# Optimization experiments

Hardware: AMD Instinct MI355X
Metric: run time of the kernel (lower is better)

## Reference

```python
import jax, jax.numpy as jnp
import numpy as np

OPS = jnp.array([[1,1,1],[1,1,-1],[1,-1,1],[1,-1,-1],[-1,1,1],[-1,1,-1],[-1,-1,1],[-1,-1,-1]], dtype=jnp.float32)  # [8,3] sign flips per eigenvector column

B, N, FN, FE, E = 1, 512, 8, 1, 32
D0 = 6 + FN  # layer-0 node embedding dim: framed (x,v) = 6 dims + node features


def setup_inputs() -> dict:
    key = jax.random.key(0)
    ks = jax.random.split(key, 24)
    rn = lambda k, shp, s=0.1: jax.random.normal(k, shp, jnp.float32) * s
    inp = {
        'node_feat': jax.random.normal(ks[0], (B, N, FN), jnp.float32),
        'edge_feat': jax.random.normal(ks[1], (B, N, N, FE), jnp.float32),
        'x': jax.random.normal(ks[2], (B, N, 3), jnp.float32),
        'v': jax.random.normal(ks[3], (B, N, 3), jnp.float32),
        # GNN layer 0 (input node dim D0)
        'e0_w1': rn(ks[4], (FE + 2 * D0, E)), 'e0_b1': jnp.zeros((E,), jnp.float32),
        'e0_w2': rn(ks[5], (E, E)), 'e0_b2': jnp.zeros((E,), jnp.float32),
        'n0_w1': rn(ks[6], (D0 + E, E)), 'n0_b1': jnp.zeros((E,), jnp.float32),
        'n0_w2': rn(ks[7], (E, E)), 'n0_b2': jnp.zeros((E,), jnp.float32),
        # GNN layer 1 (input node dim E)
        'e1_w1': rn(ks[8], (FE + 2 * E, E)), 'e1_b1': jnp.zeros((E,), jnp.float32),
        'e1_w2': rn(ks[9], (E, E)), 'e1_b2': jnp.zeros((E,), jnp.float32),
        'n1_w1': rn(ks[10], (E + E, E)), 'n1_b1': jnp.zeros((E,), jnp.float32),
        'n1_w2': rn(ks[11], (E, E)), 'n1_b2': jnp.zeros((E,), jnp.float32),
        # decoder: relu -> Linear(E,E) -> relu -> Linear(E,6)
        'dec_w1': rn(ks[12], (E, E)), 'dec_b1': jnp.zeros((E,), jnp.float32),
        'dec_w2': rn(ks[13], (E, 6)), 'dec_b2': jnp.zeros((6,), jnp.float32),
        # v_coef: relu -> Linear(E,E) -> relu -> Linear(E,1)
        'vc_w1': rn(ks[14], (E, E)), 'vc_b1': jnp.zeros((E,), jnp.float32),
        'vc_w2': rn(ks[15], (E, 1)), 'vc_b2': jnp.zeros((1,), jnp.float32),
    }
    return inp


def _gnn_layer(h, edge_feat, ew1, eb1, ew2, eb2, nw1, nb1, nw2, nb2):
    # h: [B,N,d]; edge_feat: [B,N,N,Fe]
    # Torch builds concat([edge_feat, h_j, h_i]) per (i,j) pair; we split W1 rows
    # to avoid materializing the [B,N,N,Fe+2d] concat (same math).
    Fe = edge_feat.shape[-1]
    d = h.shape[-1]
    pre_e = edge_feat @ ew1[:Fe]          # [B,N,N,E]
    pre_j = h @ ew1[Fe:Fe + d]            # [B,N,E], indexed by j
    pre_i = h @ ew1[Fe + d:]              # [B,N,E], indexed by i
    m = jax.nn.relu(pre_e + pre_j[:, None, :, :] + pre_i[:, :, None, :] + eb1)
    m = jax.nn.relu(m @ ew2 + eb2)        # [B,N,N,E]
    agg = m.sum(axis=2)                   # sum over neighbors j -> [B,N,E]
    dn = jax.nn.relu(h @ nw1[:d] + agg @ nw1[d:] + nb1)
    return dn @ nw2 + nb2                 # [B,N,E]


def reference(node_feat, edge_feat, x, v,
              e0_w1, e0_b1, e0_w2, e0_b2, n0_w1, n0_b1, n0_w2, n0_b2,
              e1_w1, e1_b1, e1_w2, e1_b2, n1_w1, n1_b1, n1_w2, n1_b2,
              dec_w1, dec_b1, dec_w2, dec_b2, vc_w1, vc_b1, vc_w2, vc_b2):
    # ---- create_frame (PCA frame averaging) ----
    center = x.mean(axis=1, keepdims=True)                 # [B,1,3]
    xc = x - center
    R = jnp.einsum('bni,bnj->bij', xc, xc)                 # [B,3,3]
    _, Vv = jnp.linalg.eigh(R)                             # eigenvectors, ascending (like torch.symeig)
    F_ops = jax.lax.stop_gradient(OPS[None, :, None, :] * Vv[:, None, :, :])  # [B,8,3,3]
    center = jax.lax.stop_gradient(center)
    xc = x - center
    fx = jnp.einsum('boji,bnj->obni', F_ops, xc)           # [8,B,N,3] (F_ops^T applied)
    fv = jnp.einsum('boji,bnj->obni', F_ops, v)            # [8,B,N,3]
    nf = jnp.broadcast_to(node_feat[None], (8,) + node_feat.shape)
    h0 = jnp.concatenate([fx, fv, nf], axis=-1)            # [8,B,N,6+FN]

    l0 = (e0_w1, e0_b1, e0_w2, e0_b2, n0_w1, n0_b1, n0_w2, n0_b2)
    l1 = (e1_w1, e1_b1, e1_w2, e1_b2, n1_w1, n1_b1, n1_w2, n1_b2)
    frames = []
    for i in range(8):  # small fixed frame count; loop keeps N^2 intermediates per-frame
        hi = _gnn_layer(h0[i], edge_feat, *l0)
        hi = _gnn_layer(hi, edge_feat, *l1)
        frames.append(hi)
    h_out = jnp.stack(frames)                              # [8,B,N,E]

    # ---- decoder + invert_frame ----
    s = jax.nn.relu(jax.nn.relu(h_out) @ dec_w1 + dec_b1)
    spatial_out = s @ dec_w2 + dec_b2                      # [8,B,N,6]
    so = jnp.transpose(spatial_out, (1, 0, 2, 3))          # [B,8,N,6]
    dx = jnp.einsum('boij,bonj->bni', F_ops, so[..., :3]) / 8.0
    dv = jnp.einsum('boij,bonj->bni', F_ops, so[..., 3:]) / 8.0

    h_mean = h_out.mean(axis=0)                            # [B,N,E]
    coef = jax.nn.relu(jax.nn.relu(h_mean) @ vc_w1 + vc_b1) @ vc_w2 + vc_b2  # [B,N,1]
    v_out = v + dv
    x_out = x + v_out * coef + dx
    return (h_mean, edge_feat, x_out, v_out)
```

## Files before the change

### kernel.cpp

```cpp
#include <hip/hip_runtime.h>
#include <hip/hip_bf16.h>
#include <hip/hip_fp16.h>
#include <math.h>

#define NN 512

typedef _Float16 f16x8 __attribute__((ext_vector_type(8)));
typedef float    f32x4 __attribute__((ext_vector_type(4)));

__device__ __forceinline__ void compute_frame(const float* __restrict__ x,
                                              float* __restrict__ sFR,
                                              double (*red)[9]) {
    const int t = threadIdx.x;
    double s[9] = {0,0,0,0,0,0,0,0,0};
    for (int n = t; n < NN; n += 256) {
        double X = x[n*3+0], Y = x[n*3+1], Z = x[n*3+2];
        s[0]+=X; s[1]+=Y; s[2]+=Z;
        s[3]+=X*X; s[4]+=X*Y; s[5]+=X*Z; s[6]+=Y*Y; s[7]+=Y*Z; s[8]+=Z*Z;
    }
    #pragma unroll
    for (int m = 1; m < 64; m <<= 1) {
        #pragma unroll
        for (int q = 0; q < 9; ++q) s[q] += __shfl_xor(s[q], m);
    }
    const int wave = t >> 6, lane = t & 63;
    if (lane == 0) {
        #pragma unroll
        for (int q = 0; q < 9; ++q) red[wave][q] = s[q];
    }
    __syncthreads();
    if (t == 0) {
        double S[9];
        #pragma unroll
        for (int q = 0; q < 9; ++q) S[q] = red[0][q]+red[1][q]+red[2][q]+red[3][q];
        double cx = S[0]/512.0, cy = S[1]/512.0, cz = S[2]/512.0;
        double A[3][3];
        A[0][0]=S[3]-512.0*cx*cx; A[0][1]=S[4]-512.0*cx*cy; A[0][2]=S[5]-512.0*cx*cz;
        A[1][1]=S[6]-512.0*cy*cy; A[1][2]=S[7]-512.0*cy*cz; A[2][2]=S[8]-512.0*cz*cz;
        A[1][0]=A[0][1]; A[2][0]=A[0][2]; A[2][1]=A[1][2];
        double V[3][3] = {{1,0,0},{0,1,0},{0,0,1}};
        for (int sweep = 0; sweep < 8; ++sweep) {
            double off = fabs(A[0][1]) + fabs(A[0][2]) + fabs(A[1][2]);
            double dia = fabs(A[0][0]) + fabs(A[1][1]) + fabs(A[2][2]);
            if (off < 1e-14 * (dia + 1e-300)) break;
            for (int p = 0; p < 3; ++p) for (int q = p+1; q < 3; ++q) {
                double apq = A[p][q];
                if (fabs(apq) < 1e-300) continue;
                double tau = (A[q][q] - A[p][p]) / (2.0 * apq);
                double tt = (tau >= 0 ? 1.0 : -1.0) / (fabs(tau) + sqrt(1.0 + tau*tau));
                double cc = 1.0 / sqrt(1.0 + tt*tt), ss = tt * cc;
                A[p][p] = A[p][p] - tt * apq;
                A[q][q] = A[q][q] + tt * apq;
                A[p][q] = 0.0; A[q][p] = 0.0;
                for (int k = 0; k < 3; ++k) if (k != p && k != q) {
                    double akp = A[k][p], akq = A[k][q];
                    A[k][p] = cc*akp - ss*akq; A[p][k] = A[k][p];
                    A[k][q] = ss*akp + cc*akq; A[q][k] = A[k][q];
                }
                for (int k = 0; k < 3; ++k) {
                    double vkp = V[k][p], vkq = V[k][q];
                    V[k][p] = cc*vkp - ss*vkq;
                    V[k][q] = ss*vkp + cc*vkq;
                }
            }
        }
        double ev[3] = {A[0][0], A[1][1], A[2][2]};
        int idx[3] = {0,1,2};
        for (int a = 0; a < 2; ++a) for (int b = a+1; b < 3; ++b)
            if (ev[idx[b]] < ev[idx[a]]) { int tmp = idx[a]; idx[a] = idx[b]; idx[b] = tmp; }
        sFR[0] = (float)cx; sFR[1] = (float)cy; sFR[2] = (float)cz;
        for (int r = 0; r < 3; ++r)
            for (int c = 0; c < 3; ++c)
                sFR[3 + r*3 + c] = (float)V[r][idx[c]];
    }
    __syncthreads();
}

__global__ void __launch_bounds__(256) pre0_kernel(
    const float* __restrict__ x, const float* __restrict__ v,
    const float* __restrict__ nf,
    const float* __restrict__ e0w1, const float* __restrict__ e0b1,
    const float* __restrict__ e0w2, const float* __restrict__ e1w1,
    const float* __restrict__ e1w2,
    const float* __restrict__ edge,
    float* __restrict__ FRg, float* __restrict__ H0,
    _Float16* __restrict__ PJF, _Float16* __restrict__ PIH,
    _Float16* __restrict__ WEH0, _Float16* __restrict__ WEH1,
    _Float16* __restrict__ W2F0, _Float16* __restrict__ W2F1,
    float* __restrict__ out_edge)
{
    __shared__ double red[4][9];
    __shared__ float sFR[12];
    const int t = threadIdx.x;
    const int b = blockIdx.x;

    compute_frame(x, sFR, red);

    ((float2*)out_edge)[b * 256 + t] = ((const float2*)edge)[b * 256 + t];

    if (b == 0) {
        const int lane = t & 63, wv = t >> 6;
        if (t < 12) FRg[t] = sFR[t];
        const int l15 = lane & 15, kb = (lane >> 4) * 8;
        if (wv == 1) {
            #pragma unroll
            for (int e = 0; e < 8; ++e) {
                W2F0[lane*16 + e]     = (_Float16)e0w2[(kb+e)*32 + l15];
                W2F0[lane*16 + 8 + e] = (_Float16)e0w2[(kb+e)*32 + l15 + 16];
            }
        } else if (wv == 2) {
            #pragma unroll
            for (int e = 0; e < 8; ++e) {
                W2F1[lane*16 + e]     = (_Float16)e1w2[(kb+e)*32 + l15];
                W2F1[lane*16 + 8 + e] = (_Float16)e1w2[(kb+e)*32 + l15 + 16];
            }
        } else if (wv == 3 && lane < 32) {
            WEH0[lane] = (_Float16)e0w1[lane];
            WEH1[lane] = (_Float16)e1w1[lane];
        }
    }

    const int c = t & 31;
    const int row = b * 8 + (t >> 5);
    const int o = row >> 9, j = row & 511;
    float hrow[14];
    float xc0 = x[j*3+0] - sFR[0], xc1 = x[j*3+1] - sFR[1], xc2 = x[j*3+2] - sFR[2];
    float v0 = v[j*3+0], v1 = v[j*3+1], v2 = v[j*3+2];
    #pragma unroll
    for (int i = 0; i < 3; ++i) {
        float sgn = ((o >> (2 - i)) & 1) ? -1.f : 1.f;
        float px = sFR[3 + 0*3 + i]*xc0 + sFR[3 + 1*3 + i]*xc1 + sFR[3 + 2*3 + i]*xc2;
        float pv = sFR[3 + 0*3 + i]*v0  + sFR[3 + 1*3 + i]*v1  + sFR[3 + 2*3 + i]*v2;
        hrow[i]     = sgn * px;
        hrow[3 + i] = sgn * pv;
    }
    #pragma unroll
    for (int k = 0; k < 8; ++k) hrow[6 + k] = nf[j*8 + k];
    if (c < 14) H0[row * 14 + c] = hrow[c];
    float pj = 0.f, pi = e0b1[c];
    #pragma unroll
    for (int k = 0; k < 14; ++k) {
        pj = fmaf(hrow[k], e0w1[(1 + k) * 32 + c], pj);
        pi = fmaf(hrow[k], e0w1[(15 + k) * 32 + c], pi);
    }
    PIH[row * 32 + c] = (_Float16)pi;
    const int fl = (j & 15) | ((c >> 3) << 4);
    PJF[(((o << 5) + (j >> 4)) * 64 + fl) * 8 + (c & 7)] = (_Float16)pj;
}

template<int D, bool NEXT>
__global__ void __launch_bounds__(256, 4) edge_kernel(
    const _Float16* __restrict__ PJF,
    const _Float16* __restrict__ PIH,
    const _Float16* __restrict__ WEH,
    const _Float16* __restrict__ W2F,
    const float* __restrict__ edge,
    const float* __restrict__ h,
    const float* __restrict__ eb2,
    const float* __restrict__ nw1,
    const float* __restrict__ nb1,
    const float* __restrict__ nw2,
    const float* __restrict__ nb2,
    float* __restrict__ hout,
    const float* __restrict__ ew1n,
    const float* __restrict__ eb1n,
    _Float16* __restrict__ PJFn,
    _Float16* __restrict__ PIn)
{
    const int t = threadIdx.x;
    const int wv = t >> 6, lane = t & 63;
    const int o = blockIdx.x >> 8;
    const int i0 = (blockIdx.x & 255) << 1;
    const int i = i0 + (wv & 1);
    const int jh = wv >> 1;
    const int row = (o << 9) | i;
    const int l15 = lane & 15;
    const int kbase = (lane >> 4) * 8;

    __shared__ float sAgg[4][32];

    const f16x8 pi8 = *(const f16x8*)(PIH + row * 32 + kbase);
    const f16x8 we8 = *(const f16x8*)(WEH + kbase);
    const f16x8 bfrag0 = *(const f16x8*)(W2F + lane * 16);
    const f16x8 bfrag1 = *(const f16x8*)(W2F + lane * 16 + 8);
    const float b2v0 = eb2[l15], b2v1 = eb2[l15 + 16];
    const f16x8 z8 = {0,0,0,0,0,0,0,0};
    float agg0 = 0.f, agg1 = 0.f;

    const float* edge_i = edge + (i << 9);
    const _Float16* pjf_o = PJF + (size_t)o * 16384;

    #pragma unroll
    for (int jm = 0; jm < 16; ++jm) {
        const int tile = (jh << 4) | jm;
        const f16x8 pj8 = *(const f16x8*)(pjf_o + (tile * 64 + lane) * 8);
        const _Float16 eh = (_Float16)edge_i[tile * 16 + l15];
        const f16x8 e8 = {eh, eh, eh, eh, eh, eh, eh, eh};
        f16x8 m = e8 * we8 + (pj8 + pi8);
        m = __builtin_elementwise_max(m, z8);
        f32x4 c0 = {0.f, 0.f, 0.f, 0.f};
        c0 = __builtin_amdgcn_mfma_f32_16x16x32_f16(m, bfrag0, c0, 0, 0, 0);
        #pragma unroll
        for (int r = 0; r < 4; ++r) agg0 += fmaxf(c0[r] + b2v0, 0.f);
        f32x4 c1 = {0.f, 0.f, 0.f, 0.f};
        c1 = __builtin_amdgcn_mfma_f32_16x16x32_f16(m, bfrag1, c1, 0, 0, 0);
        #pragma unroll
        for (int r = 0; r < 4; ++r) agg1 += fmaxf(c1[r] + b2v1, 0.f);
    }
    agg0 += __shfl_xor(agg0, 16); agg0 += __shfl_xor(agg0, 32);
    agg1 += __shfl_xor(agg1, 16); agg1 += __shfl_xor(agg1, 32);
    if (lane < 16) { sAgg[wv][l15] = agg0; sAgg[wv][16 + l15] = agg1; }
    __syncthreads();
    if (wv >= 2) return;

    const int c2 = lane & 31;
    const float red2 = sAgg[wv][c2] + sAgg[wv + 2][c2];
    const float* hr = h + row * D;
    float acc = nb1[c2];
    #pragma unroll
    for (int k = 0; k < D; ++k) acc = fmaf(hr[k], nw1[k * 32 + c2], acc);
    #pragma unroll
    for (int k = 0; k < 32; ++k)
        acc = fmaf(__shfl(red2, k, 32), nw1[(D + k) * 32 + c2], acc);
    const float dn = fmaxf(acc, 0.f);
    float outv = nb2[c2];
    #pragma unroll
    for (int k = 0; k < 32; ++k)
        outv = fmaf(__shfl(dn, k, 32), nw2[k * 32 + c2], outv);
    if (lane < 32) hout[row * 32 + c2] = outv;

    if (NEXT) {
        float pj1 = 0.f, pi1 = eb1n[c2];
        #pragma unroll
        for (int k = 0; k < 32; ++k) {
            const float hk = __shfl(outv, k, 32);
            pj1 = fmaf(hk, ew1n[(1 + k) * 32 + c2], pj1);
            pi1 = fmaf(hk, ew1n[(33 + k) * 32 + c2], pi1);
        }
        if (lane < 32) {
            PIn[row * 32 + c2] = (_Float16)pi1;
            const int fl = (i & 15) | ((c2 >> 3) << 4);
            PJFn[(((o << 5) + (i >> 4)) * 64 + fl) * 8 + (c2 & 7)] = (_Float16)pj1;
        }
    }
}

__global__ void __launch_bounds__(256) decfinal_kernel(
    const float* __restrict__ h2,
    const float* __restrict__ w1, const float* __restrict__ b1,
    const float* __restrict__ w2,
    const float* __restrict__ b2,
    const float* __restrict__ x, const float* __restrict__ v,
    const float* __restrict__ FR,
    const float* __restrict__ vw1, const float* __restrict__ vb1,
    const float* __restrict__ vw2, const float* __restrict__ vb2,
    float* __restrict__ out_hmean, float* __restrict__ out_x,
    float* __restrict__ out_v)
{
    const int n = blockIdx.x;
    const int t = threadIdx.x;
    const int wv = t >> 6, lane = t & 63;
    const int c = lane & 31;
    __shared__ float sSo[8][6];

    #pragma unroll
    for (int q = 0; q < 2; ++q) {
        const int o = (wv << 1) | q;
        const int row = (o << 9) | n;
        float rh = fmaxf(h2[row * 32 + c], 0.f);
        float acc = b1[c];
        #pragma unroll
        for (int k = 0; k < 32; ++k)
            acc = fmaf(__shfl(rh, k, 32), w1[k * 32 + c], acc);
        float s = fmaxf(acc, 0.f);
        #pragma unroll
        for (int m = 0; m < 6; ++m) {
            float p = s * w2[c * 6 + m];
            p += __shfl_xor(p, 1); p += __shfl_xor(p, 2); p += __shfl_xor(p, 4);
            p += __shfl_xor(p, 8); p += __shfl_xor(p, 16);
            if (lane == 0) sSo[o][m] = p + b2[m];
        }
    }
    __syncthreads();
    if (wv) return;

    float hm = 0.f;
    #pragma unroll
    for (int o = 0; o < 8; ++o) hm += h2[((o << 9) | n) * 32 + c];
    hm *= 0.125f;
    if (lane < 32) out_hmean[n * 32 + c] = hm;
    float rh = fmaxf(hm, 0.f);
    float acc = vb1[c];
    #pragma unroll
    for (int k = 0; k < 32; ++k)
        acc = fmaf(__shfl(rh, k, 32), vw1[k * 32 + c], acc);
    float t1 = fmaxf(acc, 0.f);
    float p = t1 * vw2[c];
    p += __shfl_xor(p, 1); p += __shfl_xor(p, 2); p += __shfl_xor(p, 4);
    p += __shfl_xor(p, 8); p += __shfl_xor(p, 16);
    float coef = p + vb2[0];
    if (lane < 3) {
        int i = lane;
        float dx = 0.f, dv = 0.f;
        #pragma unroll
        for (int o = 0; o < 8; ++o) {
            #pragma unroll
            for (int j = 0; j < 3; ++j) {
                float sgn = ((o >> (2 - j)) & 1) ? -1.f : 1.f;
                float f = sgn * FR[3 + i * 3 + j];
                dx = fmaf(f, sSo[o][j], dx);
                dv = fmaf(f, sSo[o][3 + j], dv);
            }
        }
        dx *= 0.125f; dv *= 0.125f;
        float vout = v[n * 3 + i] + dv;
        out_v[n * 3 + i] = vout;
        out_x[n * 3 + i] = x[n * 3 + i] + vout * coef + dx;
    }
}

extern "C" void kernel_launch(void* const* d_in, const int* in_sizes, int n_in,
                              void* d_out, int out_size, void* d_ws, size_t ws_size,
                              hipStream_t stream) {
    const float* node_feat = (const float*)d_in[0];
    const float* edge      = (const float*)d_in[1];
    const float* x         = (const float*)d_in[2];
    const float* v         = (const float*)d_in[3];
    const float* e0_w1 = (const float*)d_in[4];
    const float* e0_b1 = (const float*)d_in[5];
    const float* e0_w2 = (const float*)d_in[6];
    const float* e0_b2 = (const float*)d_in[7];
    const float* n0_w1 = (const float*)d_in[8];
    const float* n0_b1 = (const float*)d_in[9];
    const float* n0_w2 = (const float*)d_in[10];
    const float* n0_b2 = (const float*)d_in[11];
    const float* e1_w1 = (const float*)d_in[12];
    const float* e1_b1 = (const float*)d_in[13];
    const float* e1_w2 = (const float*)d_in[14];
    const float* e1_b2 = (const float*)d_in[15];
    const float* n1_w1 = (const float*)d_in[16];
    const float* n1_b1 = (const float*)d_in[17];
    const float* n1_w2 = (const float*)d_in[18];
    const float* n1_b2 = (const float*)d_in[19];
    const float* dec_w1 = (const float*)d_in[20];
    const float* dec_b1 = (const float*)d_in[21];
    const float* dec_w2 = (const float*)d_in[22];
    const float* dec_b2 = (const float*)d_in[23];
    const float* vc_w1 = (const float*)d_in[24];
    const float* vc_b1 = (const float*)d_in[25];
    const float* vc_w2 = (const float*)d_in[26];
    const float* vc_b2 = (const float*)d_in[27];

    char* wsb = (char*)d_ws;
    float* out = (float*)d_out;

    float*    FR   = (float*)wsb;
    float*    H0   = (float*)(wsb + 256);
    float*    HA   = (float*)(wsb + 256 + 229376);
    float*    HB   = (float*)(wsb + 256 + 229376 + 524288);
    char*     p    = wsb + 256 + 229376 + 524288 + 524288;
    _Float16* PJF0 = (_Float16*)p;            p += 262144;
    _Float16* PIH0 = (_Float16*)p;            p += 262144;
    _Float16* PJF1 = (_Float16*)p;            p += 262144;
    _Float16* PIH1 = (_Float16*)p;            p += 262144;
    _Float16* WEH0 = (_Float16*)p;            p += 256;
    _Float16* WEH1 = (_Float16*)p;            p += 256;
    _Float16* W2F0 = (_Float16*)p;            p += 2048;
    _Float16* W2F1 = (_Float16*)p;            p += 2048;

    pre0_kernel<<<512, 256, 0, stream>>>(x, v, node_feat,
                                         e0_w1, e0_b1, e0_w2, e1_w1, e1_w2,
                                         edge, FR, H0, PJF0, PIH0,
                                         WEH0, WEH1, W2F0, W2F1, out + 16384);
    edge_kernel<14, true><<<2048, 256, 0, stream>>>(
        PJF0, PIH0, WEH0, W2F0, edge, H0, e0_b2, n0_w1, n0_b1, n0_w2, n0_b2,
        HA, e1_w1, e1_b1, PJF1, PIH1);
    edge_kernel<32, false><<<2048, 256, 0, stream>>>(
        PJF1, PIH1, WEH1, W2F1, edge, HA, e1_b2, n1_w1, n1_b1, n1_w2, n1_b2,
        HB, nullptr, nullptr, nullptr, nullptr);
    decfinal_kernel<<<512, 256, 0, stream>>>(HB, dec_w1, dec_b1, dec_w2, dec_b2,
                                             x, v, FR, vc_w1, vc_b1, vc_w2, vc_b2,
                                             out, out + 278528, out + 280064);
}
```

Measured before the change: 154.9 us.

## Fuse all stages into one persistent kernel with software grid barriers

Replaces the four kernel launches with one 512-block kernel whose stages are separated by an atomic-counter grid barrier, removing launch gaps and inter-kernel drain. Each wave now handles two node rows over all 512 neighbours, sharing the PJF loads between them instead of splitting neighbours across waves and reducing through LDS. The barrier relies on all 512 blocks being resident at once (launch bounds of 3 blocks per CU), so it can deadlock if they are not co-resident. It also leaves fewer blocks in flight for latency hiding during the edge phases.

Result: slower. 366.8 us (+136.7%).

```diff
diff --git a/kernel.cpp b/kernel.cpp
--- a/kernel.cpp
+++ b/kernel.cpp
@@ -1,12 +1,53 @@
 #include <hip/hip_runtime.h>
-#include <hip/hip_bf16.h>
 #include <hip/hip_fp16.h>
 #include <math.h>
 
 #define NN 512
+#define NBLK 512
 
 typedef _Float16 f16x8 __attribute__((ext_vector_type(8)));
 typedef float    f32x4 __attribute__((ext_vector_type(4)));
+
+struct Params {
+    const float *x, *v, *nf;
+    const float *e0w1, *e0b1, *e0w2, *e0b2;
+    const float *n0w1, *n0b1, *n0w2, *n0b2;
+    const float *e1w1, *e1b1, *e1w2, *e1b2;
+    const float *n1w1, *n1b1, *n1w2, *n1b2;
+    const float *dw1, *db1, *dw2, *db2;
+    const float *vw1, *vb1, *vw2, *vb2;
+    const float *edge;
+    float *FR, *H0, *HA, *HB;
+    _Float16 *PJF0, *PIH0, *PJF1, *PIH1;
+    _Float16 *WEH0, *WEH1, *W2F0, *W2F1;
+    float *out_hmean, *out_edge, *out_x, *out_v;
+};
+
+__device__ unsigned g_bar_cnt = 0;
+__device__ unsigned g_bar_gen = 0;
+
+__device__ __forceinline__ void grid_sync() {
+    __syncthreads();
+    if (threadIdx.x == 0) {
+        __threadfence();
+        unsigned my = __hip_atomic_load(&g_bar_gen, __ATOMIC_RELAXED,
+                                        __HIP_MEMORY_SCOPE_AGENT);
+        unsigned prev = __hip_atomic_fetch_add(&g_bar_cnt, 1u, __ATOMIC_ACQ_REL,
+                                               __HIP_MEMORY_SCOPE_AGENT);
+        if (prev == (unsigned)(NBLK - 1)) {
+            __hip_atomic_store(&g_bar_cnt, 0u, __ATOMIC_RELAXED,
+                               __HIP_MEMORY_SCOPE_AGENT);
+            __hip_atomic_store(&g_bar_gen, my + 1u, __ATOMIC_RELEASE,
+                               __HIP_MEMORY_SCOPE_AGENT);
+        } else {
+            while (__hip_atomic_load(&g_bar_gen, __ATOMIC_RELAXED,
+                                     __HIP_MEMORY_SCOPE_AGENT) == my)
+                __builtin_amdgcn_s_sleep(2);
+        }
+        __threadfence();
+    }
+    __syncthreads();
+}
 
 __device__ __forceinline__ void compute_frame(const float* __restrict__ x,
                                               float* __restrict__ sFR,
@@ -76,80 +117,56 @@
     __syncthreads();
 }
 
-__global__ void __launch_bounds__(256) pre0_kernel(
-    const float* __restrict__ x, const float* __restrict__ v,
-    const float* __restrict__ nf,
-    const float* __restrict__ e0w1, const float* __restrict__ e0b1,
-    const float* __restrict__ e0w2, const float* __restrict__ e1w1,
-    const float* __restrict__ e1w2,
-    const float* __restrict__ edge,
-    float* __restrict__ FRg, float* __restrict__ H0,
-    _Float16* __restrict__ PJF, _Float16* __restrict__ PIH,
-    _Float16* __restrict__ WEH0, _Float16* __restrict__ WEH1,
-    _Float16* __restrict__ W2F0, _Float16* __restrict__ W2F1,
-    float* __restrict__ out_edge)
+template<int D, bool NEXT>
+__device__ __forceinline__ void node_tail(
+    const int row, const float agg0, const float agg1,
+    const float* __restrict__ h,
+    const float* __restrict__ nw1, const float* __restrict__ nb1,
+    const float* __restrict__ nw2, const float* __restrict__ nb2,
+    float* __restrict__ hout,
+    const float* __restrict__ ew1n, const float* __restrict__ eb1n,
+    _Float16* __restrict__ PJFn, _Float16* __restrict__ PIn)
 {
-    __shared__ double red[4][9];
-    __shared__ float sFR[12];
-    const int t = threadIdx.x;
-    const int b = blockIdx.x;
-
-    compute_frame(x, sFR, red);
-
-    ((float2*)out_edge)[b * 256 + t] = ((const float2*)edge)[b * 256 + t];
-
-    if (b == 0) {
-        const int lane = t & 63, wv = t >> 6;
-        if (t < 12) FRg[t] = sFR[t];
-        const int l15 = lane & 15, kb = (lane >> 4) * 8;
-        if (wv == 1) {
-            #pragma unroll
-            for (int e = 0; e < 8; ++e) {
-                W2F0[lane*16 + e]     = (_Float16)e0w2[(kb+e)*32 + l15];
-                W2F0[lane*16 + 8 + e] = (_Float16)e0w2[(kb+e)*32 + l15 + 16];
-            }
-        } else if (wv == 2) {
-            #pragma unroll
-            for (int e = 0; e < 8; ++e) {
-                W2F1[lane*16 + e]     = (_Float16)e1w2[(kb+e)*32 + l15];
-                W2F1[lane*16 + 8 + e] = (_Float16)e1w2[(kb+e)*32 + l15 + 16];
-            }
-        } else if (wv == 3 && lane < 32) {
-            WEH0[lane] = (_Float16)e0w1[lane];
-            WEH1[lane] = (_Float16)e1w1[lane];
-        }
-    }
-
-    const int c = t & 31;
-    const int row = b * 8 + (t >> 5);
-    const int o = row >> 9, j = row & 511;
-    float hrow[14];
-    float xc0 = x[j*3+0] - sFR[0], xc1 = x[j*3+1] - sFR[1], xc2 = x[j*3+2] - sFR[2];
-    float v0 = v[j*3+0], v1 = v[j*3+1], v2 = v[j*3+2];
+    const int lane = threadIdx.x & 63;
+    const int c2 = lane & 31;
+    const float* hr = h + row * D;
+    float acc = nb1[c2];
     #pragma unroll
-    for (int i = 0; i < 3; ++i) {
-        float sgn = ((o >> (2 - i)) & 1) ? -1.f : 1.f;
-        float px = sFR[3 + 0*3 + i]*xc0 + sFR[3 + 1*3 + i]*xc1 + sFR[3 + 2*3 + i]*xc2;
-        float pv = sFR[3 + 0*3 + i]*v0  + sFR[3 + 1*3 + i]*v1  + sFR[3 + 2*3 + i]*v2;
-        hrow[i]     = sgn * px;
-        hrow[3 + i] = sgn * pv;
-    }
+    for (int k = 0; k < D; ++k) acc = fmaf(hr[k], nw1[k * 32 + c2], acc);
     #pragma unroll
-    for (int k = 0; k < 8; ++k) hrow[6 + k] = nf[j*8 + k];
-    if (c < 14) H0[row * 14 + c] = hrow[c];
-    float pj = 0.f, pi = e0b1[c];
+    for (int k = 0; k < 16; ++k)
+        acc = fmaf(__shfl(agg0, k, 32), nw1[(D + k) * 32 + c2], acc);
     #pragma unroll
-    for (int k = 0; k < 14; ++k) {
-        pj = fmaf(hrow[k], e0w1[(1 + k) * 32 + c], pj);
-        pi = fmaf(hrow[k], e0w1[(15 + k) * 32 + c], pi);
-    }
-    PIH[row * 32 + c] = (_Float16)pi;
-    const int fl = (j & 15) | ((c >> 3) << 4);
-    PJF[(((o << 5) + (j >> 4)) * 64 + fl) * 8 + (c & 7)] = (_Float16)pj;
+    for (int k = 0; k < 16; ++k)
+        acc = fmaf(__shfl(agg1, k, 32), nw1[(D + 16 + k) * 32 + c2], acc);
+    const float dn = fmaxf(acc, 0.f);
+    float outv = nb2[c2];
+    #pragma unroll
+    for (int k = 0; k < 32; ++k)
+        outv = fmaf(__shfl(dn, k, 32), nw2[k * 32 + c2], outv);
+    if (lane < 32) hout[row * 32 + c2] = outv;
+
+    if (NEXT) {
+        float pj1 = 0.f, pi1 = eb1n[c2];
+        #pragma unroll
+        for (int k = 0; k < 32; ++k) {
+            const float hk = __shfl(outv, k, 32);
+            pj1 = fmaf(hk, ew1n[(1 + k) * 32 + c2], pj1);
+            pi1 = fmaf(hk, ew1n[(33 + k) * 32 + c2], pi1);
+        }
+        if (lane < 32) {
+            PIn[row * 32 + c2] = (_Float16)pi1;
+            const int i = row & 511;
+            const int o = row >> 9;
+            const int fl = (i & 15) | ((c2 >> 3) << 4);
+            PJFn[(((o << 5) + (i >> 4)) * 64 + fl) * 8 + (c2 & 7)] = (_Float16)pj1;
+        }
+    }
 }
 
 template<int D, bool NEXT>
-__global__ void __launch_bounds__(256, 4) edge_kernel(
+__device__ __forceinline__ void edge_phase2(
+    const int o, const int i0,
     const _Float16* __restrict__ PJF,
     const _Float16* __restrict__ PIH,
     const _Float16* __restrict__ WEH,
@@ -157,228 +174,259 @@
     const float* __restrict__ edge,
     const float* __restrict__ h,
     const float* __restrict__ eb2,
-    const float* __restrict__ nw1,
-    const float* __restrict__ nb1,
-    const float* __restrict__ nw2,
-    const float* __restrict__ nb2,
+    const float* __restrict__ nw1, const float* __restrict__ nb1,
+    const float* __restrict__ nw2, const float* __restrict__ nb2,
     float* __restrict__ hout,
-    const float* __restrict__ ew1n,
-    const float* __restrict__ eb1n,
-    _Float16* __restrict__ PJFn,
-    _Float16* __restrict__ PIn)
+    const float* __restrict__ ew1n, const float* __restrict__ eb1n,
+    _Float16* __restrict__ PJFn, _Float16* __restrict__ PIn)
 {
+    const int lane = threadIdx.x & 63;
+    const int l15 = lane & 15;
+    const int kbase = (lane >> 4) * 8;
+    const int row0 = (o << 9) | i0;
+    const int row1 = row0 + 1;
+
+    const f16x8 piA = *(const f16x8*)(PIH + row0 * 32 + kbase);
+    const f16x8 piB = *(const f16x8*)(PIH + row1 * 32 + kbase);
+    const f16x8 we8 = *(const f16x8*)(WEH + kbase);
+    const f16x8 bf0 = *(const f16x8*)(W2F + lane * 16);
+    const f16x8 bf1 = *(const f16x8*)(W2F + lane * 16 + 8);
+    const float b2v0 = eb2[l15], b2v1 = eb2[l15 + 16];
+    const f16x8 z8 = {0,0,0,0,0,0,0,0};
+    float aggA0 = 0.f, aggA1 = 0.f, aggB0 = 0.f, aggB1 = 0.f;
+
+    const float* eA = edge + (i0 << 9);
+    const float* eB = eA + 512;
+    const _Float16* pjf_o = PJF + (size_t)o * 16384;
+
+    #pragma unroll 4
+    for (int tile = 0; tile < 32; ++tile) {
+        const f16x8 pj8 = *(const f16x8*)(pjf_o + (tile * 64 + lane) * 8);
+        const _Float16 ehA = (_Float16)eA[tile * 16 + l15];
+        const _Float16 ehB = (_Float16)eB[tile * 16 + l15];
+        const f16x8 eA8 = {ehA, ehA, ehA, ehA, ehA, ehA, ehA, ehA};
+        const f16x8 eB8 = {ehB, ehB, ehB, ehB, ehB, ehB, ehB, ehB};
+        f16x8 mA = eA8 * we8 + (pj8 + piA);
+        mA = __builtin_elementwise_max(mA, z8);
+        f16x8 mB = eB8 * we8 + (pj8 + piB);
+        mB = __builtin_elementwise_max(mB, z8);
+        f32x4 c;
+        c = (f32x4){0.f,0.f,0.f,0.f};
+        c = __builtin_amdgcn_mfma_f32_16x16x32_f16(mA, bf0, c, 0, 0, 0);
+        #pragma unroll
+        for (int r = 0; r < 4; ++r) aggA0 += fmaxf(c[r] + b2v0, 0.f);
+        c = (f32x4){0.f,0.f,0.f,0.f};
+        c = __builtin_amdgcn_mfma_f32_16x16x32_f16(mA, bf1, c, 0, 0, 0);
+        #pragma unroll
+        for (int r = 0; r < 4; ++r) aggA1 += fmaxf(c[r] + b2v1, 0.f);
+        c = (f32x4){0.f,0.f,0.f,0.f};
+        c = __builtin_amdgcn_mfma_f32_16x16x32_f16(mB, bf0, c, 0, 0, 0);
+        #pragma unroll
+        for (int r = 0; r < 4; ++r) aggB0 += fmaxf(c[r] + b2v0, 0.f);
+        c = (f32x4){0.f,0.f,0.f,0.f};
+        c = __builtin_amdgcn_mfma_f32_16x16x32_f16(mB, bf1, c, 0, 0, 0);
+        #pragma unroll
+        for (int r = 0; r < 4; ++r) aggB1 += fmaxf(c[r] + b2v1, 0.f);
+    }
+    aggA0 += __shfl_xor(aggA0, 16); aggA0 += __shfl_xor(aggA0, 32);
+    aggA1 += __shfl_xor(aggA1, 16); aggA1 += __shfl_xor(aggA1, 32);
+    aggB0 += __shfl_xor(aggB0, 16); aggB0 += __shfl_xor(aggB0, 32);
+    aggB1 += __shfl_xor(aggB1, 16); aggB1 += __shfl_xor(aggB1, 32);
+
+    node_tail<D, NEXT>(row0, aggA0, aggA1, h, nw1, nb1, nw2, nb2, hout,
+                       ew1n, eb1n, PJFn, PIn);
+    node_tail<D, NEXT>(row1, aggB0, aggB1, h, nw1, nb1, nw2, nb2, hout,
+                       ew1n, eb1n, PJFn, PIn);
+}
+
+__global__ void __launch_bounds__(256, 3) fused_kernel(Params p) {
+    const int b = blockIdx.x;
     const int t = threadIdx.x;
     const int wv = t >> 6, lane = t & 63;
-    const int o = blockIdx.x >> 8;
-    const int i0 = (blockIdx.x & 255) << 1;
-    const int i = i0 + (wv & 1);
-    const int jh = wv >> 1;
-    const int row = (o << 9) | i;
-    const int l15 = lane & 15;
-    const int kbase = (lane >> 4) * 8;
-
-    __shared__ float sAgg[4][32];
-
-    const f16x8 pi8 = *(const f16x8*)(PIH + row * 32 + kbase);
-    const f16x8 we8 = *(const f16x8*)(WEH + kbase);
-    const f16x8 bfrag0 = *(const f16x8*)(W2F + lane * 16);
-    const f16x8 bfrag1 = *(const f16x8*)(W2F + lane * 16 + 8);
-    const float b2v0 = eb2[l15], b2v1 = eb2[l15 + 16];
-    const f16x8 z8 = {0,0,0,0,0,0,0,0};
-    float agg0 = 0.f, agg1 = 0.f;
-
-    const float* edge_i = edge + (i << 9);
-    const _Float16* pjf_o = PJF + (size_t)o * 16384;
-
-    #pragma unroll
-    for (int jm = 0; jm < 16; ++jm) {
-        const int tile = (jh << 4) | jm;
-        const f16x8 pj8 = *(const f16x8*)(pjf_o + (tile * 64 + lane) * 8);
-        const _Float16 eh = (_Float16)edge_i[tile * 16 + l15];
-        const f16x8 e8 = {eh, eh, eh, eh, eh, eh, eh, eh};
-        f16x8 m = e8 * we8 + (pj8 + pi8);
-        m = __builtin_elementwise_max(m, z8);
-        f32x4 c0 = {0.f, 0.f, 0.f, 0.f};
-        c0 = __builtin_amdgcn_mfma_f32_16x16x32_f16(m, bfrag0, c0, 0, 0, 0);
-        #pragma unroll
-        for (int r = 0; r < 4; ++r) agg0 += fmaxf(c0[r] + b2v0, 0.f);
-        f32x4 c1 = {0.f, 0.f, 0.f, 0.f};
-        c1 = __builtin_amdgcn_mfma_f32_16x16x32_f16(m, bfrag1, c1, 0, 0, 0);
-        #pragma unroll
-        for (int r = 0; r < 4; ++r) agg1 += fmaxf(c1[r] + b2v1, 0.f);
-    }
-    agg0 += __shfl_xor(agg0, 16); agg0 += __shfl_xor(agg0, 32);
-    agg1 += __shfl_xor(agg1, 16); agg1 += __shfl_xor(agg1, 32);
-    if (lane < 16) { sAgg[wv][l15] = agg0; sAgg[wv][16 + l15] = agg1; }
-    __syncthreads();
-    if (wv >= 2) return;
-
-    const int c2 = lane & 31;
-    const float red2 = sAgg[wv][c2] + sAgg[wv + 2][c2];
-    const float* hr = h + row * D;
-    float acc = nb1[c2];
-    #pragma unroll
-    for (int k = 0; k < D; ++k) acc = fmaf(hr[k], nw1[k * 32 + c2], acc);
-    #pragma unroll
-    for (int k = 0; k < 32; ++k)
-        acc = fmaf(__shfl(red2, k, 32), nw1[(D + k) * 32 + c2], acc);
-    const float dn = fmaxf(acc, 0.f);
-    float outv = nb2[c2];
-    #pragma unroll
-    for (int k = 0; k < 32; ++k)
-        outv = fmaf(__shfl(dn, k, 32), nw2[k * 32 + c2], outv);
-    if (lane < 32) hout[row * 32 + c2] = outv;
-
-    if (NEXT) {
-        float pj1 = 0.f, pi1 = eb1n[c2];
-        #pragma unroll
-        for (int k = 0; k < 32; ++k) {
-            const float hk = __shfl(outv, k, 32);
-            pj1 = fmaf(hk, ew1n[(1 + k) * 32 + c2], pj1);
-            pi1 = fmaf(hk, ew1n[(33 + k) * 32 + c2], pi1);
-        }
-        if (lane < 32) {
-            PIn[row * 32 + c2] = (_Float16)pi1;
-            const int fl = (i & 15) | ((c2 >> 3) << 4);
-            PJFn[(((o << 5) + (i >> 4)) * 64 + fl) * 8 + (c2 & 7)] = (_Float16)pj1;
-        }
-    }
-}
-
-__global__ void __launch_bounds__(256) decfinal_kernel(
-    const float* __restrict__ h2,
-    const float* __restrict__ w1, const float* __restrict__ b1,
-    const float* __restrict__ w2,
-    const float* __restrict__ b2,
-    const float* __restrict__ x, const float* __restrict__ v,
-    const float* __restrict__ FR,
-    const float* __restrict__ vw1, const float* __restrict__ vb1,
-    const float* __restrict__ vw2, const float* __restrict__ vb2,
-    float* __restrict__ out_hmean, float* __restrict__ out_x,
-    float* __restrict__ out_v)
-{
-    const int n = blockIdx.x;
-    const int t = threadIdx.x;
-    const int wv = t >> 6, lane = t & 63;
-    const int c = lane & 31;
+
+    __shared__ double red[4][9];
+    __shared__ float sFR[12];
     __shared__ float sSo[8][6];
 
-    #pragma unroll
-    for (int q = 0; q < 2; ++q) {
-        const int o = (wv << 1) | q;
-        const int row = (o << 9) | n;
-        float rh = fmaxf(h2[row * 32 + c], 0.f);
-        float acc = b1[c];
-        #pragma unroll
-        for (int k = 0; k < 32; ++k)
-            acc = fmaf(__shfl(rh, k, 32), w1[k * 32 + c], acc);
-        float s = fmaxf(acc, 0.f);
-        #pragma unroll
-        for (int m = 0; m < 6; ++m) {
-            float p = s * w2[c * 6 + m];
-            p += __shfl_xor(p, 1); p += __shfl_xor(p, 2); p += __shfl_xor(p, 4);
-            p += __shfl_xor(p, 8); p += __shfl_xor(p, 16);
-            if (lane == 0) sSo[o][m] = p + b2[m];
-        }
-    }
-    __syncthreads();
-    if (wv) return;
-
-    float hm = 0.f;
-    #pragma unroll
-    for (int o = 0; o < 8; ++o) hm += h2[((o << 9) | n) * 32 + c];
-    hm *= 0.125f;
-    if (lane < 32) out_hmean[n * 32 + c] = hm;
-    float rh = fmaxf(hm, 0.f);
-    float acc = vb1[c];
-    #pragma unroll
-    for (int k = 0; k < 32; ++k)
-        acc = fmaf(__shfl(rh, k, 32), vw1[k * 32 + c], acc);
-    float t1 = fmaxf(acc, 0.f);
-    float p = t1 * vw2[c];
-    p += __shfl_xor(p, 1); p += __shfl_xor(p, 2); p += __shfl_xor(p, 4);
-    p += __shfl_xor(p, 8); p += __shfl_xor(p, 16);
-    float coef = p + vb2[0];
-    if (lane < 3) {
-        int i = lane;
-        float dx = 0.f, dv = 0.f;
-        #pragma unroll
-        for (int o = 0; o < 8; ++o) {
-            #pragma unroll
-            for (int j = 0; j < 3; ++j) {
-                float sgn = ((o >> (2 - j)) & 1) ? -1.f : 1.f;
-                float f = sgn * FR[3 + i * 3 + j];
-                dx = fmaf(f, sSo[o][j], dx);
-                dv = fmaf(f, sSo[o][3 + j], dv);
+    compute_frame(p.x, sFR, red);
+
+    ((float2*)p.out_edge)[b * 256 + t] = ((const float2*)p.edge)[b * 256 + t];
+
+    if (b == 0) {
+        if (t < 12) p.FR[t] = sFR[t];
+        const int l15 = lane & 15, kb = (lane >> 4) * 8;
+        if (wv == 1) {
+            #pragma unroll
+            for (int e = 0; e < 8; ++e) {
+                p.W2F0[lane*16 + e]     = (_Float16)p.e0w2[(kb+e)*32 + l15];
+                p.W2F0[lane*16 + 8 + e] = (_Float16)p.e0w2[(kb+e)*32 + l15 + 16];
             }
-        }
-        dx *= 0.125f; dv *= 0.125f;
-        float vout = v[n * 3 + i] + dv;
-        out_v[n * 3 + i] = vout;
-        out_x[n * 3 + i] = x[n * 3 + i] + vout * coef + dx;
+        } else if (wv == 2) {
+            #pragma unroll
+            for (int e = 0; e < 8; ++e) {
+                p.W2F1[lane*16 + e]     = (_Float16)p.e1w2[(kb+e)*32 + l15];
+                p.W2F1[lane*16 + 8 + e] = (_Float16)p.e1w2[(kb+e)*32 + l15 + 16];
+            }
+        } else if (wv == 3 && lane < 32) {
+            p.WEH0[lane] = (_Float16)p.e0w1[lane];
+            p.WEH1[lane] = (_Float16)p.e1w1[lane];
+        }
+    }
+
+    {
+        const int c = t & 31;
+        const int row = b * 8 + (t >> 5);
+        const int o = row >> 9, j = row & 511;
+        float hrow[14];
+        float xc0 = p.x[j*3+0] - sFR[0], xc1 = p.x[j*3+1] - sFR[1], xc2 = p.x[j*3+2] - sFR[2];
+        float v0 = p.v[j*3+0], v1 = p.v[j*3+1], v2 = p.v[j*3+2];
+        #pragma unroll
+        for (int i = 0; i < 3; ++i) {
+            float sgn = ((o >> (2 - i)) & 1) ? -1.f : 1.f;
+            float px = sFR[3 + 0*3 + i]*xc0 + sFR[3 + 1*3 + i]*xc1 + sFR[3 + 2*3 + i]*xc2;
+            float pv = sFR[3 + 0*3 + i]*v0  + sFR[3 + 1*3 + i]*v1  + sFR[3 + 2*3 + i]*v2;
+            hrow[i]     = sgn * px;
+            hrow[3 + i] = sgn * pv;
+        }
+        #pragma unroll
+        for (int k = 0; k < 8; ++k) hrow[6 + k] = p.nf[j*8 + k];
+        if (c < 14) p.H0[row * 14 + c] = hrow[c];
+        float pj = 0.f, pi = p.e0b1[c];
+        #pragma unroll
+        for (int k = 0; k < 14; ++k) {
+            pj = fmaf(hrow[k], p.e0w1[(1 + k) * 32 + c], pj);
+            pi = fmaf(hrow[k], p.e0w1[(15 + k) * 32 + c], pi);
+        }
+        p.PIH0[row * 32 + c] = (_Float16)pi;
+        const int fl = (j & 15) | ((c >> 3) << 4);
+        p.PJF0[(((o << 5) + (j >> 4)) * 64 + fl) * 8 + (c & 7)] = (_Float16)pj;
+    }
+
+    grid_sync();
+
+    {
+        const int o = b >> 6;
+        const int i0 = ((b & 63) << 3) | (wv << 1);
+        edge_phase2<14, true>(o, i0, p.PJF0, p.PIH0, p.WEH0, p.W2F0, p.edge,
+                              p.H0, p.e0b2, p.n0w1, p.n0b1, p.n0w2, p.n0b2,
+                              p.HA, p.e1w1, p.e1b1, p.PJF1, p.PIH1);
+    }
+
+    grid_sync();
+
+    {
+        const int o = b >> 6;
+        const int i0 = ((b & 63) << 3) | (wv << 1);
+        edge_phase2<32, false>(o, i0, p.PJF1, p.PIH1, p.WEH1, p.W2F1, p.edge,
+                               p.HA, p.e1b2, p.n1w1, p.n1b1, p.n1w2, p.n1b2,
+                               p.HB, nullptr, nullptr, nullptr, nullptr);
+    }
+
+    grid_sync();
+
+    {
+        const int n = b;
+        const int c = lane & 31;
+
+        #pragma unroll
+        for (int q = 0; q < 2; ++q) {
+            const int o = (wv << 1) | q;
+            const int row = (o << 9) | n;
+            float rh = fmaxf(p.HB[row * 32 + c], 0.f);
+            float acc = p.db1[c];
+            #pragma unroll
+            for (int k = 0; k < 32; ++k)
+                acc = fmaf(__shfl(rh, k, 32), p.dw1[k * 32 + c], acc);
+            float s = fmaxf(acc, 0.f);
+            #pragma unroll
+            for (int m = 0; m < 6; ++m) {
+                float pr = s * p.dw2[c * 6 + m];
+                pr += __shfl_xor(pr, 1); pr += __shfl_xor(pr, 2); pr += __shfl_xor(pr, 4);
+                pr += __shfl_xor(pr, 8); pr += __shfl_xor(pr, 16);
+                if (lane == 0) sSo[o][m] = pr + p.db2[m];
+            }
+        }
+        __syncthreads();
+        if (wv == 0) {
+            float hm = 0.f;
+            #pragma unroll
+            for (int o = 0; o < 8; ++o) hm += p.HB[((o << 9) | n) * 32 + c];
+            hm *= 0.125f;
+            if (lane < 32) p.out_hmean[n * 32 + c] = hm;
+            float rh = fmaxf(hm, 0.f);
+            float acc = p.vb1[c];
+            #pragma unroll
+            for (int k = 0; k < 32; ++k)
+                acc = fmaf(__shfl(rh, k, 32), p.vw1[k * 32 + c], acc);
+            float t1 = fmaxf(acc, 0.f);
+            float pr = t1 * p.vw2[c];
+            pr += __shfl_xor(pr, 1); pr += __shfl_xor(pr, 2); pr += __shfl_xor(pr, 4);
+            pr += __shfl_xor(pr, 8); pr += __shfl_xor(pr, 16);
+            float coef = pr + p.vb2[0];
+            if (lane < 3) {
+                int i = lane;
+                float dx = 0.f, dv = 0.f;
+                #pragma unroll
+                for (int o = 0; o < 8; ++o) {
+                    #pragma unroll
+                    for (int j = 0; j < 3; ++j) {
+                        float sgn = ((o >> (2 - j)) & 1) ? -1.f : 1.f;
+                        float f = sgn * p.FR[3 + i * 3 + j];
+                        dx = fmaf(f, sSo[o][j], dx);
+                        dv = fmaf(f, sSo[o][3 + j], dv);
+                    }
+                }
+                dx *= 0.125f; dv *= 0.125f;
+                float vout = p.v[n * 3 + i] + dv;
+                p.out_v[n * 3 + i] = vout;
+                p.out_x[n * 3 + i] = p.x[n * 3 + i] + vout * coef + dx;
+            }
+        }
     }
 }
 
 extern "C" void kernel_launch(void* const* d_in, const int* in_sizes, int n_in,
                               void* d_out, int out_size, void* d_ws, size_t ws_size,
                               hipStream_t stream) {
-    const float* node_feat = (const float*)d_in[0];
-    const float* edge      = (const float*)d_in[1];
-    const float* x         = (const float*)d_in[2];
-    const float* v         = (const float*)d_in[3];
-    const float* e0_w1 = (const float*)d_in[4];
-    const float* e0_b1 = (const float*)d_in[5];
-    const float* e0_w2 = (const float*)d_in[6];
-    const float* e0_b2 = (const float*)d_in[7];
-    const float* n0_w1 = (const float*)d_in[8];
-    const float* n0_b1 = (const float*)d_in[9];
-    const float* n0_w2 = (const float*)d_in[10];
-    const float* n0_b2 = (const float*)d_in[11];
-    const float* e1_w1 = (const float*)d_in[12];
-    const float* e1_b1 = (const float*)d_in[13];
-    const float* e1_w2 = (const float*)d_in[14];
-    const float* e1_b2 = (const float*)d_in[15];
-    const float* n1_w1 = (const float*)d_in[16];
-    const float* n1_b1 = (const float*)d_in[17];
-    const float* n1_w2 = (const float*)d_in[18];
-    const float* n1_b2 = (const float*)d_in[19];
-    const float* dec_w1 = (const float*)d_in[20];
-    const float* dec_b1 = (const float*)d_in[21];
-    const float* dec_w2 = (const float*)d_in[22];
-    const float* dec_b2 = (const float*)d_in[23];
-    const float* vc_w1 = (const float*)d_in[24];
-    const float* vc_b1 = (const float*)d_in[25];
-    const float* vc_w2 = (const float*)d_in[26];
-    const float* vc_b2 = (const float*)d_in[27];
-
     char* wsb = (char*)d_ws;
     float* out = (float*)d_out;
 
-    float*    FR   = (float*)wsb;
-    float*    H0   = (float*)(wsb + 256);
-    float*    HA   = (float*)(wsb + 256 + 229376);
-    float*    HB   = (float*)(wsb + 256 + 229376 + 524288);
-    char*     p    = wsb + 256 + 229376 + 524288 + 524288;
-    _Float16* PJF0 = (_Float16*)p;            p += 262144;
-    _Float16* PIH0 = (_Float16*)p;            p += 262144;
-    _Float16* PJF1 = (_Float16*)p;            p += 262144;
-    _Float16* PIH1 = (_Float16*)p;            p += 262144;
-    _Float16* WEH0 = (_Float16*)p;            p += 256;
-    _Float16* WEH1 = (_Float16*)p;            p += 256;
-    _Float16* W2F0 = (_Float16*)p;            p += 2048;
-    _Float16* W2F1 = (_Float16*)p;            p += 2048;
-
-    pre0_kernel<<<512, 256, 0, stream>>>(x, v, node_feat,
-                                         e0_w1, e0_b1, e0_w2, e1_w1, e1_w2,
-                                         edge, FR, H0, PJF0, PIH0,
-                                         WEH0, WEH1, W2F0, W2F1, out + 16384);
-    edge_kernel<14, true><<<2048, 256, 0, stream>>>(
-        PJF0, PIH0, WEH0, W2F0, edge, H0, e0_b2, n0_w1, n0_b1, n0_w2, n0_b2,
-        HA, e1_w1, e1_b1, PJF1, PIH1);
-    edge_kernel<32, false><<<2048, 256, 0, stream>>>(
-        PJF1, PIH1, WEH1, W2F1, edge, HA, e1_b2, n1_w1, n1_b1, n1_w2, n1_b2,
-        HB, nullptr, nullptr, nullptr, nullptr);
-    decfinal_kernel<<<512, 256, 0, stream>>>(HB, dec_w1, dec_b1, dec_w2, dec_b2,
-                                             x, v, FR, vc_w1, vc_b1, vc_w2, vc_b2,
-                                             out, out + 278528, out + 280064);
-}
+    Params p;
+    p.nf   = (const float*)d_in[0];
+    p.edge = (const float*)d_in[1];
+    p.x    = (const float*)d_in[2];
+    p.v    = (const float*)d_in[3];
+    p.e0w1 = (const float*)d_in[4];  p.e0b1 = (const float*)d_in[5];
+    p.e0w2 = (const float*)d_in[6];  p.e0b2 = (const float*)d_in[7];
+    p.n0w1 = (const float*)d_in[8];  p.n0b1 = (const float*)d_in[9];
+    p.n0w2 = (const float*)d_in[10]; p.n0b2 = (const float*)d_in[11];
+    p.e1w1 = (const float*)d_in[12]; p.e1b1 = (const float*)d_in[13];
+    p.e1w2 = (const float*)d_in[14]; p.e1b2 = (const float*)d_in[15];
+    p.n1w1 = (const float*)d_in[16]; p.n1b1 = (const float*)d_in[17];
+    p.n1w2 = (const float*)d_in[18]; p.n1b2 = (const float*)d_in[19];
+    p.dw1  = (const float*)d_in[20]; p.db1  = (const float*)d_in[21];
+    p.dw2  = (const float*)d_in[22]; p.db2  = (const float*)d_in[23];
+    p.vw1  = (const float*)d_in[24]; p.vb1  = (const float*)d_in[25];
+    p.vw2  = (const float*)d_in[26]; p.vb2  = (const float*)d_in[27];
+
+    p.FR = (float*)wsb;
+    p.H0 = (float*)(wsb + 256);
+    p.HA = (float*)(wsb + 256 + 229376);
+    p.HB = (float*)(wsb + 256 + 229376 + 524288);
+    char* q = wsb + 256 + 229376 + 524288 + 524288;
+    p.PJF0 = (_Float16*)q; q += 262144;
+    p.PIH0 = (_Float16*)q; q += 262144;
+    p.PJF1 = (_Float16*)q; q += 262144;
+    p.PIH1 = (_Float16*)q; q += 262144;
+    p.WEH0 = (_Float16*)q; q += 256;
+    p.WEH1 = (_Float16*)q; q += 256;
+    p.W2F0 = (_Float16*)q; q += 2048;
+    p.W2F1 = (_Float16*)q; q += 2048;
+
+    p.out_hmean = out;
+    p.out_edge  = out + 16384;
+    p.out_x     = out + 278528;
+    p.out_v     = out + 280064;
+
+    fused_kernel<<<dim3(NBLK), dim3(256), 0, stream>>>(p);
+}
```

## Use fp32 Jacobi eigen-solve, hoist edge copy, split node MLP K across half-waves

Applied to the files above, without the earlier changes.

The serial single-thread 3x3 Jacobi eigen-decomposition now runs in float instead of double, which cuts latency on the critical path of every block. The edge-feature copy is moved ahead of the frame computation so its memory traffic overlaps the reduction. The per-row node MLP and next-layer projections now split the K dimension between the two 32-lane halves of the wave and combine the partial sums with a cross-half shuffle, halving the serial FMA chain length. Float Jacobi lowers the precision of the eigenvectors, which risks sign or ordering differences for near-degenerate eigenvalues.

Measured after the change: 156.0 us. No clear change (+0.7%).

```diff
diff --git a/kernel.cpp b/kernel.cpp
--- a/kernel.cpp
+++ b/kernel.cpp
@@ -34,44 +34,44 @@
         #pragma unroll
         for (int q = 0; q < 9; ++q) S[q] = red[0][q]+red[1][q]+red[2][q]+red[3][q];
         double cx = S[0]/512.0, cy = S[1]/512.0, cz = S[2]/512.0;
-        double A[3][3];
-        A[0][0]=S[3]-512.0*cx*cx; A[0][1]=S[4]-512.0*cx*cy; A[0][2]=S[5]-512.0*cx*cz;
-        A[1][1]=S[6]-512.0*cy*cy; A[1][2]=S[7]-512.0*cy*cz; A[2][2]=S[8]-512.0*cz*cz;
+        float A[3][3], V[3][3] = {{1,0,0},{0,1,0},{0,0,1}};
+        A[0][0]=(float)(S[3]-512.0*cx*cx); A[0][1]=(float)(S[4]-512.0*cx*cy);
+        A[0][2]=(float)(S[5]-512.0*cx*cz); A[1][1]=(float)(S[6]-512.0*cy*cy);
+        A[1][2]=(float)(S[7]-512.0*cy*cz); A[2][2]=(float)(S[8]-512.0*cz*cz);
         A[1][0]=A[0][1]; A[2][0]=A[0][2]; A[2][1]=A[1][2];
-        double V[3][3] = {{1,0,0},{0,1,0},{0,0,1}};
         for (int sweep = 0; sweep < 8; ++sweep) {
-            double off = fabs(A[0][1]) + fabs(A[0][2]) + fabs(A[1][2]);
-            double dia = fabs(A[0][0]) + fabs(A[1][1]) + fabs(A[2][2]);
-            if (off < 1e-14 * (dia + 1e-300)) break;
+            float off = fabsf(A[0][1]) + fabsf(A[0][2]) + fabsf(A[1][2]);
+            float dia = fabsf(A[0][0]) + fabsf(A[1][1]) + fabsf(A[2][2]);
+            if (off < 1e-7f * (dia + 1e-30f)) break;
             for (int p = 0; p < 3; ++p) for (int q = p+1; q < 3; ++q) {
-                double apq = A[p][q];
-                if (fabs(apq) < 1e-300) continue;
-                double tau = (A[q][q] - A[p][p]) / (2.0 * apq);
-                double tt = (tau >= 0 ? 1.0 : -1.0) / (fabs(tau) + sqrt(1.0 + tau*tau));
-                double cc = 1.0 / sqrt(1.0 + tt*tt), ss = tt * cc;
+                float apq = A[p][q];
+                if (fabsf(apq) < 1e-30f) continue;
+                float tau = (A[q][q] - A[p][p]) / (2.0f * apq);
+                float tt = (tau >= 0.f ? 1.0f : -1.0f) / (fabsf(tau) + sqrtf(1.0f + tau*tau));
+                float cc = 1.0f / sqrtf(1.0f + tt*tt), ss = tt * cc;
                 A[p][p] = A[p][p] - tt * apq;
                 A[q][q] = A[q][q] + tt * apq;
-                A[p][q] = 0.0; A[q][p] = 0.0;
+                A[p][q] = 0.0f; A[q][p] = 0.0f;
                 for (int k = 0; k < 3; ++k) if (k != p && k != q) {
-                    double akp = A[k][p], akq = A[k][q];
+                    float akp = A[k][p], akq = A[k][q];
                     A[k][p] = cc*akp - ss*akq; A[p][k] = A[k][p];
                     A[k][q] = ss*akp + cc*akq; A[q][k] = A[k][q];
                 }
                 for (int k = 0; k < 3; ++k) {
-                    double vkp = V[k][p], vkq = V[k][q];
+                    float vkp = V[k][p], vkq = V[k][q];
                     V[k][p] = cc*vkp - ss*vkq;
                     V[k][q] = ss*vkp + cc*vkq;
                 }
             }
         }
-        double ev[3] = {A[0][0], A[1][1], A[2][2]};
+        float ev[3] = {A[0][0], A[1][1], A[2][2]};
         int idx[3] = {0,1,2};
         for (int a = 0; a < 2; ++a) for (int b = a+1; b < 3; ++b)
             if (ev[idx[b]] < ev[idx[a]]) { int tmp = idx[a]; idx[a] = idx[b]; idx[b] = tmp; }
         sFR[0] = (float)cx; sFR[1] = (float)cy; sFR[2] = (float)cz;
         for (int r = 0; r < 3; ++r)
             for (int c = 0; c < 3; ++c)
-                sFR[3 + r*3 + c] = (float)V[r][idx[c]];
+                sFR[3 + r*3 + c] = V[r][idx[c]];
     }
     __syncthreads();
 }
@@ -94,12 +94,12 @@
     const int t = threadIdx.x;
     const int b = blockIdx.x;
 
+    ((float2*)out_edge)[b * 256 + t] = ((const float2*)edge)[b * 256 + t];
+
     compute_frame(x, sFR, red);
 
-    ((float2*)out_edge)[b * 256 + t] = ((const float2*)edge)[b * 256 + t];
-
+    const int lane = t & 63, wv = t >> 6;
     if (b == 0) {
-        const int lane = t & 63, wv = t >> 6;
         if (t < 12) FRg[t] = sFR[t];
         const int l15 = lane & 15, kb = (lane >> 4) * 8;
         if (wv == 1) {
@@ -214,29 +214,44 @@
     if (wv >= 2) return;
 
     const int c2 = lane & 31;
+    const int hf = lane >> 5;
+    const int kb = hf << 4;
     const float red2 = sAgg[wv][c2] + sAgg[wv + 2][c2];
     const float* hr = h + row * D;
-    float acc = nb1[c2];
-    #pragma unroll
-    for (int k = 0; k < D; ++k) acc = fmaf(hr[k], nw1[k * 32 + c2], acc);
-    #pragma unroll
-    for (int k = 0; k < 32; ++k)
+    constexpr int DH = D / 2;
+    float acc = hf ? 0.f : nb1[c2];
+    #pragma unroll
+    for (int kk = 0; kk < DH; ++kk) {
+        const int k = hf * DH + kk;
+        acc = fmaf(hr[k], nw1[k * 32 + c2], acc);
+    }
+    #pragma unroll
+    for (int kk = 0; kk < 16; ++kk) {
+        const int k = kb + kk;
         acc = fmaf(__shfl(red2, k, 32), nw1[(D + k) * 32 + c2], acc);
+    }
+    acc += __shfl_xor(acc, 32);
     const float dn = fmaxf(acc, 0.f);
-    float outv = nb2[c2];
-    #pragma unroll
-    for (int k = 0; k < 32; ++k)
+    float outv = hf ? 0.f : nb2[c2];
+    #pragma unroll
+    for (int kk = 0; kk < 16; ++kk) {
+        const int k = kb + kk;
         outv = fmaf(__shfl(dn, k, 32), nw2[k * 32 + c2], outv);
+    }
+    outv += __shfl_xor(outv, 32);
     if (lane < 32) hout[row * 32 + c2] = outv;
 
     if (NEXT) {
-        float pj1 = 0.f, pi1 = eb1n[c2];
-        #pragma unroll
-        for (int k = 0; k < 32; ++k) {
+        float pj1 = 0.f, pi1 = hf ? 0.f : eb1n[c2];
+        #pragma unroll
+        for (int kk = 0; kk < 16; ++kk) {
+            const int k = kb + kk;
             const float hk = __shfl(outv, k, 32);
             pj1 = fmaf(hk, ew1n[(1 + k) * 32 + c2], pj1);
             pi1 = fmaf(hk, ew1n[(33 + k) * 32 + c2], pi1);
         }
+        pj1 += __shfl_xor(pj1, 32);
+        pi1 += __shfl_xor(pi1, 32);
         if (lane < 32) {
             PIn[row * 32 + c2] = (_Float16)pi1;
             const int fl = (i & 15) | ((c2 >> 3) << 4);
```
